# Optimization experiments

Hardware: AMD Instinct MI355X
Metric: run time of the kernel (lower is better)

Reference implementation:

```python
import jax, jax.numpy as jnp
import numpy as np

D_MODEL = 1024
N_HEADS = 16
D_V = D_MODEL // N_HEADS  # 64


def setup_inputs() -> dict:
    key = jax.random.key(0)
    k1, k2, k3, k4, k5, k6 = jax.random.split(key, 6)
    N, L = 2, 2048
    return {
        "queries": jax.random.normal(k1, (N, L, D_MODEL), jnp.float32),
        "keys": jax.random.normal(k2, (N, L, D_MODEL), jnp.float32),
        "values": jax.random.normal(k3, (N, L, D_MODEL), jnp.float32),
        # key-padding mask, 0 = masked out (broadcast over heads and queries)
        "mask": jax.random.randint(k4, (N, 1, 1, L), 0, 2).astype(jnp.int32),
        # torch nn.Linear(d_model, d_model): weight [out, in], bias [out]
        "fc_w": jax.random.normal(k5, (D_MODEL, D_MODEL), jnp.float32) / np.sqrt(D_MODEL).astype(np.float32),
        "fc_b": jax.random.normal(k6, (D_MODEL,), jnp.float32) * 0.01,
    }


def reference(queries, keys, values, mask, fc_w, fc_b):
    N, Lq, _ = queries.shape
    Lk = keys.shape[1]
    # NOTE: the source defines Q/K/V Linear layers but never applies them in forward.
    q = queries.reshape(N, Lq, N_HEADS, D_V).transpose(0, 2, 1, 3)  # [N,H,Lq,Dv]
    k = keys.reshape(N, Lk, N_HEADS, D_V)                            # [N,Lk,H,Dv]
    v = values.reshape(N, Lk, N_HEADS, D_V)                          # [N,Lk,H,Dv]
    energy = jnp.einsum('nhqd,nkhd->nhqk', q, k)                     # QK^T
    energy = jnp.where(mask == 0, -jnp.inf, energy)                  # masked_fill
    # faithful to source: scale by sqrt(d_model), applied after masking
    attn = jax.nn.softmax(energy / jnp.sqrt(jnp.float32(D_MODEL)), axis=-1)
    out = jnp.einsum('nhqk,nkhd->nqhd', attn, v).reshape(N, Lq, N_HEADS * D_V)
    return out @ fc_w.T + fc_b
```

## Files before the change

kernel.cpp:

```cpp
#include <hip/hip_runtime.h>
#include <hip/hip_bf16.h>

#define SEQL 2048
#define DMODEL 1024

typedef short bf16x8 __attribute__((ext_vector_type(8)));
typedef short bf16x4 __attribute__((ext_vector_type(4)));
typedef float f32x4 __attribute__((ext_vector_type(4)));
typedef unsigned short u16;

__device__ __forceinline__ u16 f2bf(float f) {
    union { float f; unsigned u; } v; v.f = f;
    unsigned r = v.u + 0x7FFFu + ((v.u >> 16) & 1u);
    return (u16)(r >> 16);
}

__device__ __forceinline__ float fexp2(float x) {
#if __has_builtin(__builtin_amdgcn_exp2f)
    return __builtin_amdgcn_exp2f(x);
#else
    return exp2f(x);
#endif
}

#define SCALE2 0.04508422f

__device__ __forceinline__ void async16(u16* lds, const u16* g) {
    __builtin_amdgcn_global_load_lds(
        (const __attribute__((address_space(1))) unsigned int*)g,
        (__attribute__((address_space(3))) unsigned int*)lds,
        16, 0, 0);
}


#define TSTR 72

__global__ __launch_bounds__(256) void pack_all(
    const float* __restrict__ kg, const float* __restrict__ wg,
    const float* __restrict__ vg, const int* __restrict__ mg,
    u16* __restrict__ kb, u16* __restrict__ wb, u16* __restrict__ vtb,
    float* __restrict__ maskf)
{
    __shared__ __align__(16) u16 T[64 * TSTR];
    const int b = blockIdx.x, t = threadIdx.x;
    u16 o[8];
    if (b < 2048) {
        const int e0 = (b * 256 + t) * 8;
        const int n = e0 >> 21;
        const int s = (e0 >> 10) & 2047;
        const int dm = e0 & 1023, h = dm >> 6, d0 = dm & 63;
        const float4 x0 = *(const float4*)(kg + e0);
        const float4 x1 = *(const float4*)(kg + e0 + 4);
        o[0]=f2bf(x0.x); o[1]=f2bf(x0.y); o[2]=f2bf(x0.z); o[3]=f2bf(x0.w);
        o[4]=f2bf(x1.x); o[5]=f2bf(x1.y); o[6]=f2bf(x1.z); o[7]=f2bf(x1.w);
        const int kt = s >> 6, st = (s >> 4) & 3, m = s & 15;
        const int f = d0 >> 5, qd = (d0 >> 3) & 3;
        u16* dst = kb + ((size_t)((n * 16 + h) * 32 + kt)) * 4096
                      + (st * 2 + f) * 512 + (m + 16 * qd) * 8;
        *(bf16x8*)dst = *(bf16x8*)o;
    } else if (b < 2560) {
        const int e0 = ((b - 2048) * 256 + t) * 8;
        const int col = e0 >> 10, k0 = e0 & 1023;
        const float4 x0 = *(const float4*)(wg + e0);
        const float4 x1 = *(const float4*)(wg + e0 + 4);
        o[0]=f2bf(x0.x); o[1]=f2bf(x0.y); o[2]=f2bf(x0.z); o[3]=f2bf(x0.w);
        o[4]=f2bf(x1.x); o[5]=f2bf(x1.y); o[6]=f2bf(x1.z); o[7]=f2bf(x1.w);
        const int cb = col >> 6, cj = (col >> 4) & 3, m = col & 15;
        const int kt = k0 >> 6, f = (k0 >> 5) & 1, qd = (k0 >> 3) & 3;
        u16* dst = wb + ((size_t)((cb * 16 + kt) * 8 + cj * 2 + f)) * 512
                      + (m + 16 * qd) * 8;
        *(bf16x8*)dst = *(bf16x8*)o;
    } else if (b < 3584) {
        const int bb = b - 2560;
        const int kt = bb & 31, h = (bb >> 5) & 15, n = bb >> 9;
        {
            const int s = t >> 2, d0 = (t & 3) * 16;
            const float* src = vg + ((size_t)(n * SEQL + kt * 64 + s) * DMODEL) + h * 64 + d0;
            u16 w16[16];
            #pragma unroll
            for (int j = 0; j < 16; ++j) w16[j] = f2bf(src[j]);
            *(bf16x8*)&T[s * TSTR + d0]     = *(bf16x8*)&w16[0];
            *(bf16x8*)&T[s * TSTR + d0 + 8] = *(bf16x8*)&w16[8];
        }
        __syncthreads();
        {
            const int d = t >> 2, k0 = (t & 3) * 16;
            u16 w16[16];
            #pragma unroll
            for (int j = 0; j < 16; ++j) w16[j] = T[(k0 + j) * TSTR + d];
            const int t4 = d >> 4, dr = d & 15;
            u16* base = vtb + ((size_t)((n * 16 + h) * 32 + kt)) * 4096;
            #pragma unroll
            for (int g = 0; g < 2; ++g) {
                const int key0 = k0 + g * 8;
                const int kk = key0 >> 5, qk = (key0 >> 3) & 3;
                *(bf16x8*)(base + (t4 * 2 + kk) * 512 + (dr + 16 * qk) * 8)
                    = *(bf16x8*)&w16[g * 8];
            }
        }
    } else {
        #pragma unroll
        for (int i = 0; i < 16; ++i) {
            const int idx = t * 16 + i;
            maskf[idx] = mg[idx] ? 0.0f : -1.0e5f;
        }
    }
}

__global__ __launch_bounds__(512, 4) void attn_fused(
    const float* __restrict__ qg, const u16* __restrict__ kb,
    const u16* __restrict__ vtb, const float* __restrict__ maskf,
    u16* __restrict__ xb)
{
    __shared__ __align__(16) u16 SM[20480];

    const int b = blockIdx.x;
    const int xcd = b & 7;
    const int j = b >> 3;
    const int qblk = j & 15;
    const int hn = xcd * 4 + (j >> 4);
    const int h = hn & 15;
    const int n = hn >> 4;

    const int tid = threadIdx.x;
    const int wave = tid >> 6, lane = tid & 63;
    const int half = wave >> 2, w4 = wave & 3;
    const int lrow = lane & 15, quad = lane >> 4;
    const int q0 = qblk * 128;

    u16* const P_lds = SM + wave * 2048;

    const u16* ksrc = kb  + ((size_t)(n * 16 + h)) * 131072 + (size_t)half * 65536;
    const u16* vsrc = vtb + ((size_t)(n * 16 + h)) * 131072 + (size_t)half * 65536;
    const float* mrow = maskf + n * SEQL + half * 1024;

    bf16x8 qf[2][2];
    #pragma unroll
    for (int qi = 0; qi < 2; ++qi) {
        const float* qp = qg + ((size_t)(n * SEQL + q0 + w4 * 32 + qi * 16 + lrow) * DMODEL) + h * 64 + quad * 8;
        #pragma unroll
        for (int f = 0; f < 2; ++f) {
            const float4 a = *(const float4*)(qp + f * 32);
            const float4 c = *(const float4*)(qp + f * 32 + 4);
            u16* dst = (u16*)&qf[qi][f];
            dst[0]=f2bf(a.x); dst[1]=f2bf(a.y); dst[2]=f2bf(a.z); dst[3]=f2bf(a.w);
            dst[4]=f2bf(c.x); dst[5]=f2bf(c.y); dst[6]=f2bf(c.z); dst[7]=f2bf(c.w);
        }
    }

    bf16x8 onesf;
    #pragma unroll
    for (int jj = 0; jj < 8; ++jj) ((u16*)&onesf)[jj] = 0x3F80;

    f32x4 oacc[2][4];
    f32x4 lacc[2];
    #pragma unroll
    for (int qi = 0; qi < 2; ++qi) {
        lacc[qi] = (f32x4){0.f, 0.f, 0.f, 0.f};
        #pragma unroll
        for (int t4 = 0; t4 < 4; ++t4) oacc[qi][t4] = (f32x4){0.f, 0.f, 0.f, 0.f};
    }

    for (int i = 0; i < 16; ++i) {
        const u16* kp = ksrc + (size_t)i * 4096 + lane * 8;
        const u16* vp = vsrc + (size_t)i * 4096 + lane * 8;
        bf16x8 kf[8], vf[8];
        #pragma unroll
        for (int f = 0; f < 8; ++f) kf[f] = *(const bf16x8*)(kp + f * 512);
        #pragma unroll
        for (int f = 0; f < 8; ++f) vf[f] = *(const bf16x8*)(vp + f * 512);

        #pragma unroll
        for (int st = 0; st < 4; ++st) {
            const f32x4 mv = *(const f32x4*)&mrow[i * 64 + st * 16 + quad * 4];
            const int kk = st >> 1;
            const int qk = (st & 1) * 2 + (quad >> 1);
            const int j0 = (quad & 1) * 4;
            #pragma unroll
            for (int qi = 0; qi < 2; ++qi) {
                f32x4 sa = (f32x4){0.f, 0.f, 0.f, 0.f};
                sa = __builtin_amdgcn_mfma_f32_16x16x32_bf16(kf[st * 2 + 0], qf[qi][0], sa, 0, 0, 0);
                sa = __builtin_amdgcn_mfma_f32_16x16x32_bf16(kf[st * 2 + 1], qf[qi][1], sa, 0, 0, 0);
                float e0v = fexp2(fmaf(sa[0], SCALE2, mv[0]));
                float e1v = fexp2(fmaf(sa[1], SCALE2, mv[1]));
                float e2v = fexp2(fmaf(sa[2], SCALE2, mv[2]));
                float e3v = fexp2(fmaf(sa[3], SCALE2, mv[3]));
                __hip_bfloat162 h0 = __float22bfloat162_rn(make_float2(e0v, e1v));
                __hip_bfloat162 h1 = __float22bfloat162_rn(make_float2(e2v, e3v));
                union { unsigned u[2]; bf16x4 v; } pk;
                pk.u[0] = *(unsigned*)&h0;
                pk.u[1] = *(unsigned*)&h1;
                *(bf16x4*)&P_lds[(qi * 2 + kk) * 512 + (lrow + 16 * qk) * 8 + j0] = pk.v;
            }
        }
        asm volatile("s_waitcnt lgkmcnt(0)" ::: "memory");

        #pragma unroll
        for (int qi = 0; qi < 2; ++qi) {
            const bf16x8 pf0 = *(const bf16x8*)&P_lds[(qi * 2 + 0) * 512 + lane * 8];
            const bf16x8 pf1 = *(const bf16x8*)&P_lds[(qi * 2 + 1) * 512 + lane * 8];
            lacc[qi] = __builtin_amdgcn_mfma_f32_16x16x32_bf16(pf0, onesf, lacc[qi], 0, 0, 0);
            lacc[qi] = __builtin_amdgcn_mfma_f32_16x16x32_bf16(pf1, onesf, lacc[qi], 0, 0, 0);
            #pragma unroll
            for (int t4 = 0; t4 < 4; ++t4) {
                oacc[qi][t4] = __builtin_amdgcn_mfma_f32_16x16x32_bf16(pf0, vf[t4 * 2 + 0], oacc[qi][t4], 0, 0, 0);
                oacc[qi][t4] = __builtin_amdgcn_mfma_f32_16x16x32_bf16(pf1, vf[t4 * 2 + 1], oacc[qi][t4], 0, 0, 0);
            }
        }
    }

    __syncthreads();
    float* const Pf = (float*)SM;
    float* const Lf = (float*)(SM + 16384);
    if (half) {
        float* dst = Pf + (size_t)(w4 * 64 + lane) * 32;
        float* ld  = Lf + (size_t)(w4 * 64 + lane) * 8;
        #pragma unroll
        for (int qi = 0; qi < 2; ++qi) {
            *(f32x4*)(ld + qi * 4) = lacc[qi];
            #pragma unroll
            for (int t4 = 0; t4 < 4; ++t4)
                *(f32x4*)(dst + qi * 16 + t4 * 4) = oacc[qi][t4];
        }
    }
    __syncthreads();
    if (!half) {
        const float* src = Pf + (size_t)(w4 * 64 + lane) * 32;
        const float* ls  = Lf + (size_t)(w4 * 64 + lane) * 8;
        #pragma unroll
        for (int qi = 0; qi < 2; ++qi) {
            lacc[qi] += *(const f32x4*)(ls + qi * 4);
            #pragma unroll
            for (int t4 = 0; t4 < 4; ++t4)
                oacc[qi][t4] += *(const f32x4*)(src + qi * 16 + t4 * 4);
        }
        #pragma unroll
        for (int qi = 0; qi < 2; ++qi)
            #pragma unroll
            for (int r = 0; r < 4; ++r) {
                const float rinv = 1.0f / lacc[qi][r];
                const int row = n * SEQL + q0 + w4 * 32 + qi * 16 + quad * 4 + r;
                const int rb = row >> 7, rt = (row >> 4) & 7, m = row & 15;
                #pragma unroll
                for (int t4 = 0; t4 < 4; ++t4) {
                    const int f = t4 >> 1;
                    const int qd = (t4 & 1) * 2 + (lrow >> 3);
                    xb[((size_t)((rb * 16 + h) * 16 + rt * 2 + f)) * 512
                       + (m + 16 * qd) * 8 + (lrow & 7)] = f2bf(oacc[qi][t4][r] * rinv);
                }
            }
    }
}

__global__ __launch_bounds__(256) void fc_kernel(
    const u16* __restrict__ xb, const u16* __restrict__ wb,
    const float* __restrict__ bias, float* __restrict__ out)
{
    __shared__ __align__(16) u16 SM[24576];
    u16* const X_lds = SM;
    u16* const W_lds = SM + 16384;

    const int blk = blockIdx.x;
    const int cb = blk & 15, rb = blk >> 4;
    const int tid = threadIdx.x;
    const int wave = tid >> 6, lane = tid & 63;
    const int lrow = lane & 15, quad = lane >> 4;

    const u16* xs0 = xb + ((size_t)rb * 16) * 8192;
    const u16* ws0 = wb + ((size_t)cb * 16) * 4096;

    f32x4 acc[2][4];
    #pragma unroll
    for (int ri = 0; ri < 2; ++ri)
        #pragma unroll
        for (int cj = 0; cj < 4; ++cj) acc[ri][cj] = (f32x4){0.f, 0.f, 0.f, 0.f};

    {
        #pragma unroll
        for (int i = 0; i < 4; ++i) {
            const int ch = tid + i * 256;
            async16(&X_lds[ch * 8], xs0 + ch * 8);
        }
        #pragma unroll
        for (int i = 0; i < 2; ++i) {
            const int ch = tid + i * 256;
            async16(&W_lds[ch * 8], ws0 + ch * 8);
        }
    }
    __syncthreads();

    for (int kt = 0; kt < 16; ++kt) {
        const int cur = kt & 1;
        const u16* const Xc = X_lds + cur * 8192;
        const u16* const Wc = W_lds + cur * 4096;

        if (kt + 1 < 16) {
            const int nxt = cur ^ 1;
            const u16* xs = xs0 + (size_t)(kt + 1) * 8192;
            const u16* ws = ws0 + (size_t)(kt + 1) * 4096;
            #pragma unroll
            for (int i = 0; i < 4; ++i) {
                const int ch = tid + i * 256;
                async16(&X_lds[nxt * 8192 + ch * 8], xs + ch * 8);
            }
            #pragma unroll
            for (int i = 0; i < 2; ++i) {
                const int ch = tid + i * 256;
                async16(&W_lds[nxt * 4096 + ch * 8], ws + ch * 8);
            }
        }

        bf16x8 af[2][2];
        #pragma unroll
        for (int ri = 0; ri < 2; ++ri) {
            af[ri][0] = *(const bf16x8*)&Xc[((wave * 2 + ri) * 2 + 0) * 512 + lane * 8];
            af[ri][1] = *(const bf16x8*)&Xc[((wave * 2 + ri) * 2 + 1) * 512 + lane * 8];
        }
        #pragma unroll
        for (int cj = 0; cj < 4; ++cj) {
            const bf16x8 bf0 = *(const bf16x8*)&Wc[(cj * 2 + 0) * 512 + lane * 8];
            const bf16x8 bf1 = *(const bf16x8*)&Wc[(cj * 2 + 1) * 512 + lane * 8];
            #pragma unroll
            for (int ri = 0; ri < 2; ++ri) {
                acc[ri][cj] = __builtin_amdgcn_mfma_f32_16x16x32_bf16(af[ri][0], bf0, acc[ri][cj], 0, 0, 0);
                acc[ri][cj] = __builtin_amdgcn_mfma_f32_16x16x32_bf16(af[ri][1], bf1, acc[ri][cj], 0, 0, 0);
            }
        }

        __syncthreads();
    }

    const int row0 = rb * 128, col0 = cb * 64;
    #pragma unroll
    for (int ri = 0; ri < 2; ++ri)
        #pragma unroll
        for (int cj = 0; cj < 4; ++cj) {
            const int col = col0 + cj * 16 + lrow;
            const float bv = bias[col];
            #pragma unroll
            for (int r = 0; r < 4; ++r)
                out[(size_t)(row0 + wave * 32 + ri * 16 + quad * 4 + r) * DMODEL + col] = acc[ri][cj][r] + bv;
        }
}

extern "C" void kernel_launch(void* const* d_in, const int* in_sizes, int n_in,
                              void* d_out, int out_size, void* d_ws, size_t ws_size,
                              hipStream_t stream) {
    const float* q   = (const float*)d_in[0];
    const float* k   = (const float*)d_in[1];
    const float* v   = (const float*)d_in[2];
    const int*   m   = (const int*)d_in[3];
    const float* fcw = (const float*)d_in[4];
    const float* fcb = (const float*)d_in[5];
    float* out = (float*)d_out;

    char* ws = (char*)d_ws;
    u16*   kbuf  = (u16*)(ws);
    u16*   vtbuf = (u16*)(ws + (8u  << 20));
    u16*   wbuf  = (u16*)(ws + (16u << 20));
    u16*   xbuf  = (u16*)(ws + (18u << 20));
    float* maskf = (float*)(ws + (26u << 20));

    pack_all<<<dim3(3585), dim3(256), 0, stream>>>(k, fcw, v, m, kbuf, wbuf, vtbuf, maskf);
    attn_fused<<<dim3(512), dim3(512), 0, stream>>>(q, kbuf, vtbuf, maskf, xbuf);
    fc_kernel<<<dim3(512), dim3(256), 0, stream>>>(xbuf, wbuf, fcb, out);
}
```

Baseline: 173.5 us.

## Halve query tile per attention block to double grid size and occupancy

Each attention block now handles 64 query rows instead of 128, with each wave owning one 16-row tile instead of two. The grid doubles to 1024 blocks, LDS use halves, and launch bounds request 8 blocks per CU so more waves are resident. The cost is that each K/V tile loaded from global memory now feeds half as many queries, doubling K/V traffic and making the kernel rely more on cache.

```diff
diff --git a/kernel.cpp b/kernel.cpp
--- a/kernel.cpp
+++ b/kernel.cpp
@@ -107,18 +107,18 @@
     }
 }
 
-__global__ __launch_bounds__(512, 4) void attn_fused(
+__global__ __launch_bounds__(512, 8) void attn_fused(
     const float* __restrict__ qg, const u16* __restrict__ kb,
     const u16* __restrict__ vtb, const float* __restrict__ maskf,
     u16* __restrict__ xb)
 {
-    __shared__ __align__(16) u16 SM[20480];
+    __shared__ __align__(16) u16 SM[10240];
 
     const int b = blockIdx.x;
     const int xcd = b & 7;
     const int j = b >> 3;
-    const int qblk = j & 15;
-    const int hn = xcd * 4 + (j >> 4);
+    const int qblk = j & 31;
+    const int hn = xcd * 4 + (j >> 5);
     const int h = hn & 15;
     const int n = hn >> 4;
 
@@ -126,23 +126,22 @@
     const int wave = tid >> 6, lane = tid & 63;
     const int half = wave >> 2, w4 = wave & 3;
     const int lrow = lane & 15, quad = lane >> 4;
-    const int q0 = qblk * 128;
-
-    u16* const P_lds = SM + wave * 2048;
+    const int q0 = qblk * 64;
+
+    u16* const P_lds = SM + wave * 1024;
 
     const u16* ksrc = kb  + ((size_t)(n * 16 + h)) * 131072 + (size_t)half * 65536;
     const u16* vsrc = vtb + ((size_t)(n * 16 + h)) * 131072 + (size_t)half * 65536;
     const float* mrow = maskf + n * SEQL + half * 1024;
 
-    bf16x8 qf[2][2];
-    #pragma unroll
-    for (int qi = 0; qi < 2; ++qi) {
-        const float* qp = qg + ((size_t)(n * SEQL + q0 + w4 * 32 + qi * 16 + lrow) * DMODEL) + h * 64 + quad * 8;
+    bf16x8 qf[2];
+    {
+        const float* qp = qg + ((size_t)(n * SEQL + q0 + w4 * 16 + lrow) * DMODEL) + h * 64 + quad * 8;
         #pragma unroll
         for (int f = 0; f < 2; ++f) {
             const float4 a = *(const float4*)(qp + f * 32);
             const float4 c = *(const float4*)(qp + f * 32 + 4);
-            u16* dst = (u16*)&qf[qi][f];
+            u16* dst = (u16*)&qf[f];
             dst[0]=f2bf(a.x); dst[1]=f2bf(a.y); dst[2]=f2bf(a.z); dst[3]=f2bf(a.w);
             dst[4]=f2bf(c.x); dst[5]=f2bf(c.y); dst[6]=f2bf(c.z); dst[7]=f2bf(c.w);
         }
@@ -152,14 +151,10 @@
     #pragma unroll
     for (int jj = 0; jj < 8; ++jj) ((u16*)&onesf)[jj] = 0x3F80;
 
-    f32x4 oacc[2][4];
-    f32x4 lacc[2];
+    f32x4 oacc[4];
+    f32x4 lacc = (f32x4){0.f, 0.f, 0.f, 0.f};
     #pragma unroll
-    for (int qi = 0; qi < 2; ++qi) {
-        lacc[qi] = (f32x4){0.f, 0.f, 0.f, 0.f};
-        #pragma unroll
-        for (int t4 = 0; t4 < 4; ++t4) oacc[qi][t4] = (f32x4){0.f, 0.f, 0.f, 0.f};
-    }
+    for (int t4 = 0; t4 < 4; ++t4) oacc[t4] = (f32x4){0.f, 0.f, 0.f, 0.f};
 
     for (int i = 0; i < 16; ++i) {
         const u16* kp = ksrc + (size_t)i * 4096 + lane * 8;
@@ -176,79 +171,65 @@
             const int kk = st >> 1;
             const int qk = (st & 1) * 2 + (quad >> 1);
             const int j0 = (quad & 1) * 4;
-            #pragma unroll
-            for (int qi = 0; qi < 2; ++qi) {
-                f32x4 sa = (f32x4){0.f, 0.f, 0.f, 0.f};
-                sa = __builtin_amdgcn_mfma_f32_16x16x32_bf16(kf[st * 2 + 0], qf[qi][0], sa, 0, 0, 0);
-                sa = __builtin_amdgcn_mfma_f32_16x16x32_bf16(kf[st * 2 + 1], qf[qi][1], sa, 0, 0, 0);
-                float e0v = fexp2(fmaf(sa[0], SCALE2, mv[0]));
-                float e1v = fexp2(fmaf(sa[1], SCALE2, mv[1]));
-                float e2v = fexp2(fmaf(sa[2], SCALE2, mv[2]));
-                float e3v = fexp2(fmaf(sa[3], SCALE2, mv[3]));
-                __hip_bfloat162 h0 = __float22bfloat162_rn(make_float2(e0v, e1v));
-                __hip_bfloat162 h1 = __float22bfloat162_rn(make_float2(e2v, e3v));
-                union { unsigned u[2]; bf16x4 v; } pk;
-                pk.u[0] = *(unsigned*)&h0;
-                pk.u[1] = *(unsigned*)&h1;
-                *(bf16x4*)&P_lds[(qi * 2 + kk) * 512 + (lrow + 16 * qk) * 8 + j0] = pk.v;
-            }
+            f32x4 sa = (f32x4){0.f, 0.f, 0.f, 0.f};
+            sa = __builtin_amdgcn_mfma_f32_16x16x32_bf16(kf[st * 2 + 0], qf[0], sa, 0, 0, 0);
+            sa = __builtin_amdgcn_mfma_f32_16x16x32_bf16(kf[st * 2 + 1], qf[1], sa, 0, 0, 0);
+            float e0v = fexp2(fmaf(sa[0], SCALE2, mv[0]));
+            float e1v = fexp2(fmaf(sa[1], SCALE2, mv[1]));
+            float e2v = fexp2(fmaf(sa[2], SCALE2, mv[2]));
+            float e3v = fexp2(fmaf(sa[3], SCALE2, mv[3]));
+            __hip_bfloat162 h0 = __float22bfloat162_rn(make_float2(e0v, e1v));
+            __hip_bfloat162 h1 = __float22bfloat162_rn(make_float2(e2v, e3v));
+            union { unsigned u[2]; bf16x4 v; } pk;
+            pk.u[0] = *(unsigned*)&h0;
+            pk.u[1] = *(unsigned*)&h1;
+            *(bf16x4*)&P_lds[kk * 512 + (lrow + 16 * qk) * 8 + j0] = pk.v;
         }
         asm volatile("s_waitcnt lgkmcnt(0)" ::: "memory");
 
-        #pragma unroll
-        for (int qi = 0; qi < 2; ++qi) {
-            const bf16x8 pf0 = *(const bf16x8*)&P_lds[(qi * 2 + 0) * 512 + lane * 8];
-            const bf16x8 pf1 = *(const bf16x8*)&P_lds[(qi * 2 + 1) * 512 + lane * 8];
-            lacc[qi] = __builtin_amdgcn_mfma_f32_16x16x32_bf16(pf0, onesf, lacc[qi], 0, 0, 0);
-            lacc[qi] = __builtin_amdgcn_mfma_f32_16x16x32_bf16(pf1, onesf, lacc[qi], 0, 0, 0);
-            #pragma unroll
-            for (int t4 = 0; t4 < 4; ++t4) {
-                oacc[qi][t4] = __builtin_amdgcn_mfma_f32_16x16x32_bf16(pf0, vf[t4 * 2 + 0], oacc[qi][t4], 0, 0, 0);
-                oacc[qi][t4] = __builtin_amdgcn_mfma_f32_16x16x32_bf16(pf1, vf[t4 * 2 + 1], oacc[qi][t4], 0, 0, 0);
-            }
+        const bf16x8 pf0 = *(const bf16x8*)&P_lds[0 * 512 + lane * 8];
+        const bf16x8 pf1 = *(const bf16x8*)&P_lds[1 * 512 + lane * 8];
+        lacc = __builtin_amdgcn_mfma_f32_16x16x32_bf16(pf0, onesf, lacc, 0, 0, 0);
+        lacc = __builtin_amdgcn_mfma_f32_16x16x32_bf16(pf1, onesf, lacc, 0, 0, 0);
+        #pragma unroll
+        for (int t4 = 0; t4 < 4; ++t4) {
+            oacc[t4] = __builtin_amdgcn_mfma_f32_16x16x32_bf16(pf0, vf[t4 * 2 + 0], oacc[t4], 0, 0, 0);
+            oacc[t4] = __builtin_amdgcn_mfma_f32_16x16x32_bf16(pf1, vf[t4 * 2 + 1], oacc[t4], 0, 0, 0);
         }
     }
 
     __syncthreads();
     float* const Pf = (float*)SM;
-    float* const Lf = (float*)(SM + 16384);
+    float* const Lf = (float*)(SM + 8192);
     if (half) {
-        float* dst = Pf + (size_t)(w4 * 64 + lane) * 32;
-        float* ld  = Lf + (size_t)(w4 * 64 + lane) * 8;
-        #pragma unroll
-        for (int qi = 0; qi < 2; ++qi) {
-            *(f32x4*)(ld + qi * 4) = lacc[qi];
-            #pragma unroll
-            for (int t4 = 0; t4 < 4; ++t4)
-                *(f32x4*)(dst + qi * 16 + t4 * 4) = oacc[qi][t4];
-        }
+        float* dst = Pf + (size_t)(w4 * 64 + lane) * 16;
+        float* ld  = Lf + (size_t)(w4 * 64 + lane) * 4;
+        *(f32x4*)ld = lacc;
+        #pragma unroll
+        for (int t4 = 0; t4 < 4; ++t4)
+            *(f32x4*)(dst + t4 * 4) = oacc[t4];
     }
     __syncthreads();
     if (!half) {
-        const float* src = Pf + (size_t)(w4 * 64 + lane) * 32;
-        const float* ls  = Lf + (size_t)(w4 * 64 + lane) * 8;
-        #pragma unroll
-        for (int qi = 0; qi < 2; ++qi) {
-            lacc[qi] += *(const f32x4*)(ls + qi * 4);
-            #pragma unroll
-            for (int t4 = 0; t4 < 4; ++t4)
-                oacc[qi][t4] += *(const f32x4*)(src + qi * 16 + t4 * 4);
-        }
-        #pragma unroll
-        for (int qi = 0; qi < 2; ++qi)
-            #pragma unroll
-            for (int r = 0; r < 4; ++r) {
-                const float rinv = 1.0f / lacc[qi][r];
-                const int row = n * SEQL + q0 + w4 * 32 + qi * 16 + quad * 4 + r;
-                const int rb = row >> 7, rt = (row >> 4) & 7, m = row & 15;
-                #pragma unroll
-                for (int t4 = 0; t4 < 4; ++t4) {
-                    const int f = t4 >> 1;
-                    const int qd = (t4 & 1) * 2 + (lrow >> 3);
-                    xb[((size_t)((rb * 16 + h) * 16 + rt * 2 + f)) * 512
-                       + (m + 16 * qd) * 8 + (lrow & 7)] = f2bf(oacc[qi][t4][r] * rinv);
-                }
-            }
+        const float* src = Pf + (size_t)(w4 * 64 + lane) * 16;
+        const float* ls  = Lf + (size_t)(w4 * 64 + lane) * 4;
+        lacc += *(const f32x4*)ls;
+        #pragma unroll
+        for (int t4 = 0; t4 < 4; ++t4)
+            oacc[t4] += *(const f32x4*)(src + t4 * 4);
+        #pragma unroll
+        for (int r = 0; r < 4; ++r) {
+            const float rinv = 1.0f / lacc[r];
+            const int row = n * SEQL + q0 + w4 * 16 + quad * 4 + r;
+            const int rb = row >> 7, rt = (row >> 4) & 7, m = row & 15;
+            #pragma unroll
+            for (int t4 = 0; t4 < 4; ++t4) {
+                const int f = t4 >> 1;
+                const int qd = (t4 & 1) * 2 + (lrow >> 3);
+                xb[((size_t)((rb * 16 + h) * 16 + rt * 2 + f)) * 512
+                   + (m + 16 * qd) * 8 + (lrow & 7)] = f2bf(oacc[t4][r] * rinv);
+            }
+        }
     }
 }
 
@@ -362,6 +343,6 @@
     float* maskf = (float*)(ws + (26u << 20));
 
     pack_all<<<dim3(3585), dim3(256), 0, stream>>>(k, fcw, v, m, kbuf, wbuf, vtbuf, maskf);
-    attn_fused<<<dim3(512), dim3(512), 0, stream>>>(q, kbuf, vtbuf, maskf, xbuf);
+    attn_fused<<<dim3(1024), dim3(512), 0, stream>>>(q, kbuf, vtbuf, maskf, xbuf);
     fc_kernel<<<dim3(512), dim3(256), 0, stream>>>(xbuf, wbuf, fcb, out);
 }
```

Result: slower. 312.6 us (+80.1%).

## Split attention keys four ways per block and halve query tile to double grid

Applied to the files above, without the earlier changes.

The attention kernel now handles 64 queries per block instead of 128, with the eight waves arranged as two row groups by four key splits (512 keys each) instead of four row groups by two splits. The grid doubles to 1024 blocks and the partial output and denominator accumulators are merged through a two-step shared-memory tree reduction. The launch-bounds occupancy hint is raised from 4 to 6. The aim is more parallelism and shorter per-wave loops to hide latency. In exchange it adds extra barriers and reduction traffic, each K/V tile is re-read by twice as many blocks, and register pressure tightens under the higher occupancy target.

```diff
diff --git a/kernel.cpp b/kernel.cpp
--- a/kernel.cpp
+++ b/kernel.cpp
@@ -107,7 +107,7 @@
     }
 }
 
-__global__ __launch_bounds__(512, 4) void attn_fused(
+__global__ __launch_bounds__(512, 6) void attn_fused(
     const float* __restrict__ qg, const u16* __restrict__ kb,
     const u16* __restrict__ vtb, const float* __restrict__ maskf,
     u16* __restrict__ xb)
@@ -117,27 +117,28 @@
     const int b = blockIdx.x;
     const int xcd = b & 7;
     const int j = b >> 3;
-    const int qblk = j & 15;
-    const int hn = xcd * 4 + (j >> 4);
+    const int qblk = j & 31;
+    const int hn = xcd * 4 + (j >> 5);
     const int h = hn & 15;
     const int n = hn >> 4;
 
     const int tid = threadIdx.x;
     const int wave = tid >> 6, lane = tid & 63;
-    const int half = wave >> 2, w4 = wave & 3;
+    const int rg = wave & 1;
+    const int s = wave >> 1;
     const int lrow = lane & 15, quad = lane >> 4;
-    const int q0 = qblk * 128;
+    const int q0 = qblk * 64;
 
     u16* const P_lds = SM + wave * 2048;
 
-    const u16* ksrc = kb  + ((size_t)(n * 16 + h)) * 131072 + (size_t)half * 65536;
-    const u16* vsrc = vtb + ((size_t)(n * 16 + h)) * 131072 + (size_t)half * 65536;
-    const float* mrow = maskf + n * SEQL + half * 1024;
+    const u16* ksrc = kb  + ((size_t)(n * 16 + h)) * 131072 + (size_t)s * 32768;
+    const u16* vsrc = vtb + ((size_t)(n * 16 + h)) * 131072 + (size_t)s * 32768;
+    const float* mrow = maskf + n * SEQL + s * 512;
 
     bf16x8 qf[2][2];
     #pragma unroll
     for (int qi = 0; qi < 2; ++qi) {
-        const float* qp = qg + ((size_t)(n * SEQL + q0 + w4 * 32 + qi * 16 + lrow) * DMODEL) + h * 64 + quad * 8;
+        const float* qp = qg + ((size_t)(n * SEQL + q0 + rg * 32 + qi * 16 + lrow) * DMODEL) + h * 64 + quad * 8;
         #pragma unroll
         for (int f = 0; f < 2; ++f) {
             const float4 a = *(const float4*)(qp + f * 32);
@@ -161,7 +162,7 @@
         for (int t4 = 0; t4 < 4; ++t4) oacc[qi][t4] = (f32x4){0.f, 0.f, 0.f, 0.f};
     }
 
-    for (int i = 0; i < 16; ++i) {
+    for (int i = 0; i < 8; ++i) {
         const u16* kp = ksrc + (size_t)i * 4096 + lane * 8;
         const u16* vp = vsrc + (size_t)i * 4096 + lane * 8;
         bf16x8 kf[8], vf[8];
@@ -210,36 +211,55 @@
     }
 
     __syncthreads();
-    float* const Pf = (float*)SM;
-    float* const Lf = (float*)(SM + 16384);
-    if (half) {
-        float* dst = Pf + (size_t)(w4 * 64 + lane) * 32;
-        float* ld  = Lf + (size_t)(w4 * 64 + lane) * 8;
-        #pragma unroll
-        for (int qi = 0; qi < 2; ++qi) {
-            *(f32x4*)(ld + qi * 4) = lacc[qi];
+    float* const CB = (float*)SM;
+    if (s >= 2) {
+        float* dst = CB + ((size_t)((wave - 4) * 64 + lane)) * 40;
+        #pragma unroll
+        for (int qi = 0; qi < 2; ++qi) {
             #pragma unroll
             for (int t4 = 0; t4 < 4; ++t4)
                 *(f32x4*)(dst + qi * 16 + t4 * 4) = oacc[qi][t4];
-        }
-    }
-    __syncthreads();
-    if (!half) {
-        const float* src = Pf + (size_t)(w4 * 64 + lane) * 32;
-        const float* ls  = Lf + (size_t)(w4 * 64 + lane) * 8;
-        #pragma unroll
-        for (int qi = 0; qi < 2; ++qi) {
-            lacc[qi] += *(const f32x4*)(ls + qi * 4);
+            *(f32x4*)(dst + 32 + qi * 4) = lacc[qi];
+        }
+    }
+    __syncthreads();
+    if (s < 2) {
+        const float* src = CB + ((size_t)(wave * 64 + lane)) * 40;
+        #pragma unroll
+        for (int qi = 0; qi < 2; ++qi) {
             #pragma unroll
             for (int t4 = 0; t4 < 4; ++t4)
                 oacc[qi][t4] += *(const f32x4*)(src + qi * 16 + t4 * 4);
+            lacc[qi] += *(const f32x4*)(src + 32 + qi * 4);
+        }
+    }
+    __syncthreads();
+    if (s == 1) {
+        float* dst = CB + ((size_t)((wave - 2) * 64 + lane)) * 40;
+        #pragma unroll
+        for (int qi = 0; qi < 2; ++qi) {
+            #pragma unroll
+            for (int t4 = 0; t4 < 4; ++t4)
+                *(f32x4*)(dst + qi * 16 + t4 * 4) = oacc[qi][t4];
+            *(f32x4*)(dst + 32 + qi * 4) = lacc[qi];
+        }
+    }
+    __syncthreads();
+    if (s == 0) {
+        const float* src = CB + ((size_t)(wave * 64 + lane)) * 40;
+        #pragma unroll
+        for (int qi = 0; qi < 2; ++qi) {
+            #pragma unroll
+            for (int t4 = 0; t4 < 4; ++t4)
+                oacc[qi][t4] += *(const f32x4*)(src + qi * 16 + t4 * 4);
+            lacc[qi] += *(const f32x4*)(src + 32 + qi * 4);
         }
         #pragma unroll
         for (int qi = 0; qi < 2; ++qi)
             #pragma unroll
             for (int r = 0; r < 4; ++r) {
                 const float rinv = 1.0f / lacc[qi][r];
-                const int row = n * SEQL + q0 + w4 * 32 + qi * 16 + quad * 4 + r;
+                const int row = n * SEQL + q0 + rg * 32 + qi * 16 + quad * 4 + r;
                 const int rb = row >> 7, rt = (row >> 4) & 7, m = row & 15;
                 #pragma unroll
                 for (int t4 = 0; t4 < 4; ++t4) {
@@ -362,6 +382,6 @@
     float* maskf = (float*)(ws + (26u << 20));
 
     pack_all<<<dim3(3585), dim3(256), 0, stream>>>(k, fcw, v, m, kbuf, wbuf, vtbuf, maskf);
-    attn_fused<<<dim3(512), dim3(512), 0, stream>>>(q, kbuf, vtbuf, maskf, xbuf);
+    attn_fused<<<dim3(1024), dim3(512), 0, stream>>>(q, kbuf, vtbuf, maskf, xbuf);
     fc_kernel<<<dim3(512), dim3(256), 0, stream>>>(xbuf, wbuf, fcb, out);
 }
```

New measurement: 286.0 us. +64.8%, slower.
